# Optimization experiments

Hardware: AMD Instinct MI355X
Metric: run time of the kernel (lower is better)

The kernel has to match this reference:

```python
import jax, jax.numpy as jnp
import numpy as np

B, T, C, HEAD = 4, 4096, 1024, 64
SCALE = 1.0 / (C ** 0.5)  # module divides by embedding_size**0.5, not head_size**0.5


def setup_inputs() -> dict:
    key = jax.random.key(0)
    kx, kq, kk, kv = jax.random.split(key, 4)
    x = jax.random.normal(kx, (B, T, C), dtype=jnp.float32)
    # nn.Linear(C, head_size, bias=False) weights, stored as (C, head_size) for x @ W
    Wq = jax.random.normal(kq, (C, HEAD), dtype=jnp.float32) * (1.0 / np.sqrt(C))
    Wk = jax.random.normal(kk, (C, HEAD), dtype=jnp.float32) * (1.0 / np.sqrt(C))
    Wv = jax.random.normal(kv, (C, HEAD), dtype=jnp.float32) * (1.0 / np.sqrt(C))
    return {"x": x, "Wq": Wq, "Wk": Wk, "Wv": Wv}


def reference(x, Wq, Wk, Wv):
    q = jnp.einsum('btc,ch->bth', x, Wq)  # [B,T,HEAD]
    k = jnp.einsum('btc,ch->bth', x, Wk)
    v = jnp.einsum('btc,ch->bth', x, Wv)
    aff = jnp.einsum('bqh,bkh->bqk', q, k) * SCALE  # [B,T,T]
    causal = jnp.tril(jnp.ones((T, T), dtype=bool))
    aff = jnp.where(causal, aff, -jnp.inf)
    p = jax.nn.softmax(aff, axis=-1)  # dropout p=0.0 -> identity
    return jnp.einsum('bqk,bkh->bqh', p, v)  # [B,T,HEAD]
```

## Files before the change

kernel.cpp:

```cpp
#include <hip/hip_runtime.h>

#define T_SEQ 4096
#define NBATCH 4
#define CDIM 1024
#define NHEAD 64
#define SCALE (1.0f / 32.0f)
#define BT (NBATCH * T_SEQ)
#define NW 8

typedef __bf16 bf16x8 __attribute__((ext_vector_type(8)));
typedef float f32x4 __attribute__((ext_vector_type(4)));
typedef unsigned long long u64;

__device__ __forceinline__ unsigned short f2bf(float f) {
  union { float f; unsigned u; } x;
  x.f = f;
  unsigned r = x.u + 0x7FFFu + ((x.u >> 16) & 1u);
  return (unsigned short)(r >> 16);
}

__device__ __forceinline__ unsigned pack_bf16(float lo, float hi) {
  return (unsigned)f2bf(lo) | ((unsigned)f2bf(hi) << 16);
}

__device__ __forceinline__ f32x4 mfma16(bf16x8 a, bf16x8 b, f32x4 c) {
  return __builtin_amdgcn_mfma_f32_16x16x32_bf16(a, b, c, 0, 0, 0);
}

__device__ __forceinline__ bf16x8 ones8() {
  bf16x8 v;
  for (int j = 0; j < 8; ++j) v[j] = (__bf16)1.0f;
  return v;
}

__global__ void prep_w(const float* __restrict__ Wq, const float* __restrict__ Wk,
                       const float* __restrict__ Wv, unsigned short* __restrict__ Wt) {
  int c = blockIdx.x;
  const float* W = (c < 64) ? Wq : (c < 128) ? Wk : Wv;
  int cc = c & 63;
  float sc = (c < 64) ? SCALE : 1.0f;
  for (int k = threadIdx.x; k < CDIM; k += blockDim.x)
    Wt[c * CDIM + k] = f2bf(W[k * NHEAD + cc] * sc);
}

__global__ __launch_bounds__(256) void proj_qkv(
    const float* __restrict__ x, const unsigned short* __restrict__ Wt,
    unsigned short* __restrict__ qws, unsigned short* __restrict__ kws,
    unsigned short* __restrict__ vtws) {
  __shared__ unsigned short xlds[32][136];
  const int tid = threadIdx.x;
  const int lane = tid & 63;
  const int w = tid >> 6;
  const int g = lane >> 4;
  const int c15 = lane & 15;
  const int rb = blockIdx.x * 32;

  f32x4 acc[2][3];
  for (int i = 0; i < 2; i++)
    for (int j = 0; j < 3; j++) acc[i][j] = (f32x4){0.f, 0.f, 0.f, 0.f};

  const int sr = tid >> 3;
  const int sc = (tid & 7) * 16;
  const float* xrow = x + (size_t)(rb + sr) * CDIM + sc;

  float4 cur[4];
  for (int i = 0; i < 4; i++) cur[i] = *(const float4*)(xrow + i * 4);

  for (int k0 = 0; k0 < CDIM; k0 += 128) {
    unsigned short pk[16];
    for (int i = 0; i < 4; i++) {
      pk[i * 4 + 0] = f2bf(cur[i].x);
      pk[i * 4 + 1] = f2bf(cur[i].y);
      pk[i * 4 + 2] = f2bf(cur[i].z);
      pk[i * 4 + 3] = f2bf(cur[i].w);
    }
    *(bf16x8*)&xlds[sr][sc] = *(bf16x8*)&pk[0];
    *(bf16x8*)&xlds[sr][sc + 8] = *(bf16x8*)&pk[8];
    __syncthreads();
    if (k0 + 128 < CDIM)
      for (int i = 0; i < 4; i++)
        cur[i] = *(const float4*)(xrow + k0 + 128 + i * 4);

    for (int kk = 0; kk < 4; kk++) {
      bf16x8 a[2];
      for (int mt = 0; mt < 2; mt++)
        a[mt] = *(bf16x8*)&xlds[mt * 16 + c15][kk * 32 + g * 8];
      for (int bn = 0; bn < 3; bn++) {
        int col = w * 48 + bn * 16 + c15;
        bf16x8 bfrag =
            *(const bf16x8*)&Wt[(size_t)col * CDIM + k0 + kk * 32 + g * 8];
        for (int mt = 0; mt < 2; mt++)
          acc[mt][bn] = mfma16(a[mt], bfrag, acc[mt][bn]);
      }
    }
    __syncthreads();
  }

  for (int mt = 0; mt < 2; mt++)
    for (int bn = 0; bn < 3; bn++) {
      int col = w * 48 + bn * 16 + c15;
      int row0 = rb + mt * 16 + 4 * g;
      for (int r = 0; r < 4; r++) {
        unsigned short v = f2bf(acc[mt][bn][r]);
        int t = row0 + r;
        if (col < 64)
          qws[(size_t)t * 64 + col] = v;
        else if (col < 128)
          kws[(size_t)t * 64 + (col - 64)] = v;
        else
          vtws[(size_t)(col - 128) * BT + t] = v;
      }
    }
}

__global__ __launch_bounds__(512, 2) void attn_fwd(
    const unsigned short* __restrict__ qws, const unsigned short* __restrict__ kws,
    const unsigned short* __restrict__ vtws, float* __restrict__ out) {
  __shared__ __align__(16) char smem[NW * 8448];
  const int tid = threadIdx.x;
  const int lane = tid & 63;
  const int w = tid >> 6;
  const int g = lane >> 4;
  const int c = lane & 15;
  const int b = blockIdx.x >> 6;
  const int pi = blockIdx.x & 63;
  const size_t rowbase = (size_t)b * T_SEQ;
  char* wbase = smem + w * 8448;
  u64* pl = (u64*)wbase;
  const bf16x8 vone = ones8();

  for (int half = 0; half < 2; ++half) {
    const int qt = half ? (127 - pi) : pi;
    const int qb = qt * 32;
    const int nsteps = qt + 1;

    bf16x8 qf[2][2];
    for (int mi = 0; mi < 2; mi++)
      for (int hc = 0; hc < 2; hc++)
        qf[mi][hc] = *(const bf16x8*)&qws[(rowbase + qb + mi * 16 + c) * 64 +
                                          hc * 32 + g * 8];

    f32x4 o[2][4];
    f32x4 o5[2];
    float mrow[2];
    for (int mi = 0; mi < 2; mi++) {
      for (int nt = 0; nt < 4; nt++) o[mi][nt] = (f32x4){0.f, 0.f, 0.f, 0.f};
      o5[mi] = (f32x4){0.f, 0.f, 0.f, 0.f};
      mrow[mi] = -1e30f;
    }

    for (int st = w; st < nsteps; st += NW) {
      const int kt = st * 32;
      bf16x8 kc0[2], kc1[2], vc[4];
      for (int kn = 0; kn < 2; kn++) {
        kc0[kn] = *(const bf16x8*)&kws[(rowbase + kt + kn * 16 + c) * 64 + g * 8];
        kc1[kn] =
            *(const bf16x8*)&kws[(rowbase + kt + kn * 16 + c) * 64 + 32 + g * 8];
      }
      for (int nt = 0; nt < 4; nt++)
        vc[nt] =
            *(const bf16x8*)&vtws[(size_t)(nt * 16 + c) * BT + rowbase + kt + g * 8];

      f32x4 sv[2][2];
      for (int mi = 0; mi < 2; mi++)
        for (int kn = 0; kn < 2; kn++) {
          f32x4 z = (f32x4){0.f, 0.f, 0.f, 0.f};
          z = mfma16(kc0[kn], qf[mi][0], z);
          sv[mi][kn] = mfma16(kc1[kn], qf[mi][1], z);
        }

      if (st == nsteps - 1) {
        for (int mi = 0; mi < 2; mi++)
          for (int kn = 0; kn < 2; kn++)
            for (int r = 0; r < 4; r++) {
              int key = kt + kn * 16 + 4 * g + r;
              int qr = qb + mi * 16 + c;
              if (key > qr) sv[mi][kn][r] = -1e30f;
            }
      }

      for (int mi = 0; mi < 2; mi++) {
        float t = fmaxf(
            fmaxf(fmaxf(sv[mi][0][0], sv[mi][0][1]),
                  fmaxf(sv[mi][0][2], sv[mi][0][3])),
            fmaxf(fmaxf(sv[mi][1][0], sv[mi][1][1]),
                  fmaxf(sv[mi][1][2], sv[mi][1][3])));
        t = fmaxf(t, __shfl_xor(t, 16));
        t = fmaxf(t, __shfl_xor(t, 32));
        if (__any(t > mrow[mi] + 8.0f)) {
          float mn = fmaxf(mrow[mi], t);
          float a = __expf(mrow[mi] - mn);
          mrow[mi] = mn;
          for (int nt = 0; nt < 4; nt++) o[mi][nt] *= a;
          o5[mi] *= a;
        }
        for (int kn = 0; kn < 2; kn++)
          for (int r = 0; r < 4; r++)
            sv[mi][kn][r] = __expf(sv[mi][kn][r] - mrow[mi]);
        unsigned d0 = pack_bf16(sv[mi][0][0], sv[mi][0][1]);
        unsigned d1 = pack_bf16(sv[mi][0][2], sv[mi][0][3]);
        unsigned d2 = pack_bf16(sv[mi][1][0], sv[mi][1][1]);
        unsigned d3 = pack_bf16(sv[mi][1][2], sv[mi][1][3]);
        int row = mi * 16 + c;
        pl[row * 10 + g] = ((u64)d1 << 32) | d0;
        pl[row * 10 + 4 + g] = ((u64)d3 << 32) | d2;
      }

      asm volatile("" ::: "memory");

      for (int mi = 0; mi < 2; mi++) {
        union { u64 q[2]; bf16x8 v; } pu;
        pu.q[0] = pl[(mi * 16 + c) * 10 + 2 * g];
        pu.q[1] = pl[(mi * 16 + c) * 10 + 2 * g + 1];
        bf16x8 pa = pu.v;
        for (int nt = 0; nt < 4; nt++)
          o[mi][nt] = mfma16(vc[nt], pa, o[mi][nt]);
        o5[mi] = mfma16(vone, pa, o5[mi]);
      }
    }

    float* ow = (float*)wbase;
    float* mw = (float*)(wbase + 8192);
    float* lw = (float*)(wbase + 8320);
    for (int mi = 0; mi < 2; mi++)
      for (int nt = 0; nt < 4; nt++)
        for (int r = 0; r < 4; r++)
          ow[(mi * 16 + c) * 64 + nt * 16 + 4 * g + r] = o[mi][nt][r];
    if (g == 0)
      for (int mi = 0; mi < 2; mi++) {
        mw[mi * 16 + c] = mrow[mi];
        lw[mi * 16 + c] = o5[mi][0];
      }
    __syncthreads();

    for (int i = 0; i < 4; i++) {
      int e = tid + i * 512;
      int row = e >> 6;
      int d = e & 63;
      float M = -1e30f;
      for (int ww = 0; ww < NW; ww++)
        M = fmaxf(M, ((const float*)(smem + ww * 8448 + 8192))[row]);
      float L = 0.f, O = 0.f;
      for (int ww = 0; ww < NW; ww++) {
        float mv = ((const float*)(smem + ww * 8448 + 8192))[row];
        float f = __expf(mv - M);
        L += f * ((const float*)(smem + ww * 8448 + 8320))[row];
        O += f * ((const float*)(smem + ww * 8448))[row * 64 + d];
      }
      out[(rowbase + qb + row) * 64 + d] = O / L;
    }
    __syncthreads();
  }
}

extern "C" void kernel_launch(void* const* d_in, const int* in_sizes, int n_in,
                              void* d_out, int out_size, void* d_ws, size_t ws_size,
                              hipStream_t stream) {
  const float* x = (const float*)d_in[0];
  const float* Wq = (const float*)d_in[1];
  const float* Wk = (const float*)d_in[2];
  const float* Wv = (const float*)d_in[3];
  float* out = (float*)d_out;

  char* ws = (char*)d_ws;
  unsigned short* Wt = (unsigned short*)(ws);
  unsigned short* qws = (unsigned short*)(ws + 393216);
  unsigned short* kws = (unsigned short*)(ws + 393216 + 2097152);
  unsigned short* vtws = (unsigned short*)(ws + 393216 + 2 * 2097152);

  prep_w<<<dim3(192), dim3(256), 0, stream>>>(Wq, Wk, Wv, Wt);
  proj_qkv<<<dim3(512), dim3(256), 0, stream>>>(x, Wt, qws, kws, vtws);
  attn_fwd<<<dim3(256), dim3(512), 0, stream>>>(qws, kws, vtws, out);
}
```

Baseline: 80.25 us.

## Double attention waves per block, halve projection tile, pad LDS strides

The attention kernel now runs 16 waves per block instead of 8. This splits each query tile's KV range across more waves and merges their partial softmax states through shared memory, with the output scratch stride padded to 68 and the P-tile stride changed to 9 to reduce bank conflicts. The projection kernel processes 16 rows per block instead of 32 and launches twice as many blocks for more parallelism. The risks are a costlier cross-wave merge over 16 partials, more LDS per block, and less reuse of weight fragments in the projection.

```diff
diff --git a/kernel.cpp b/kernel.cpp
--- a/kernel.cpp
+++ b/kernel.cpp
@@ -6,7 +6,9 @@
 #define NHEAD 64
 #define SCALE (1.0f / 32.0f)
 #define BT (NBATCH * T_SEQ)
-#define NW 8
+#define NW 16
+#define WREG 8960
+#define PSTR 9
 
 typedef __bf16 bf16x8 __attribute__((ext_vector_type(8)));
 typedef float f32x4 __attribute__((ext_vector_type(4)));
@@ -47,76 +49,69 @@
     const float* __restrict__ x, const unsigned short* __restrict__ Wt,
     unsigned short* __restrict__ qws, unsigned short* __restrict__ kws,
     unsigned short* __restrict__ vtws) {
-  __shared__ unsigned short xlds[32][136];
+  __shared__ unsigned short xlds[16][136];
   const int tid = threadIdx.x;
   const int lane = tid & 63;
   const int w = tid >> 6;
   const int g = lane >> 4;
   const int c15 = lane & 15;
-  const int rb = blockIdx.x * 32;
-
-  f32x4 acc[2][3];
-  for (int i = 0; i < 2; i++)
-    for (int j = 0; j < 3; j++) acc[i][j] = (f32x4){0.f, 0.f, 0.f, 0.f};
-
-  const int sr = tid >> 3;
-  const int sc = (tid & 7) * 16;
-  const float* xrow = x + (size_t)(rb + sr) * CDIM + sc;
-
-  float4 cur[4];
-  for (int i = 0; i < 4; i++) cur[i] = *(const float4*)(xrow + i * 4);
+  const int rb = blockIdx.x * 16;
+
+  f32x4 acc[3];
+  for (int j = 0; j < 3; j++) acc[j] = (f32x4){0.f, 0.f, 0.f, 0.f};
+
+  const int sr = tid >> 4;
+  const int scc = (tid & 15) * 8;
+  const float* xrow = x + (size_t)(rb + sr) * CDIM + scc;
+
+  float4 cur[2];
+  cur[0] = *(const float4*)(xrow);
+  cur[1] = *(const float4*)(xrow + 4);
 
   for (int k0 = 0; k0 < CDIM; k0 += 128) {
-    unsigned short pk[16];
-    for (int i = 0; i < 4; i++) {
-      pk[i * 4 + 0] = f2bf(cur[i].x);
-      pk[i * 4 + 1] = f2bf(cur[i].y);
-      pk[i * 4 + 2] = f2bf(cur[i].z);
-      pk[i * 4 + 3] = f2bf(cur[i].w);
-    }
-    *(bf16x8*)&xlds[sr][sc] = *(bf16x8*)&pk[0];
-    *(bf16x8*)&xlds[sr][sc + 8] = *(bf16x8*)&pk[8];
-    __syncthreads();
-    if (k0 + 128 < CDIM)
-      for (int i = 0; i < 4; i++)
-        cur[i] = *(const float4*)(xrow + k0 + 128 + i * 4);
+    unsigned short pk[8];
+    pk[0] = f2bf(cur[0].x); pk[1] = f2bf(cur[0].y);
+    pk[2] = f2bf(cur[0].z); pk[3] = f2bf(cur[0].w);
+    pk[4] = f2bf(cur[1].x); pk[5] = f2bf(cur[1].y);
+    pk[6] = f2bf(cur[1].z); pk[7] = f2bf(cur[1].w);
+    *(bf16x8*)&xlds[sr][scc] = *(bf16x8*)pk;
+    __syncthreads();
+    if (k0 + 128 < CDIM) {
+      cur[0] = *(const float4*)(xrow + k0 + 128);
+      cur[1] = *(const float4*)(xrow + k0 + 132);
+    }
 
     for (int kk = 0; kk < 4; kk++) {
-      bf16x8 a[2];
-      for (int mt = 0; mt < 2; mt++)
-        a[mt] = *(bf16x8*)&xlds[mt * 16 + c15][kk * 32 + g * 8];
+      bf16x8 a = *(bf16x8*)&xlds[c15][kk * 32 + g * 8];
       for (int bn = 0; bn < 3; bn++) {
         int col = w * 48 + bn * 16 + c15;
         bf16x8 bfrag =
             *(const bf16x8*)&Wt[(size_t)col * CDIM + k0 + kk * 32 + g * 8];
-        for (int mt = 0; mt < 2; mt++)
-          acc[mt][bn] = mfma16(a[mt], bfrag, acc[mt][bn]);
+        acc[bn] = mfma16(a, bfrag, acc[bn]);
       }
     }
     __syncthreads();
   }
 
-  for (int mt = 0; mt < 2; mt++)
-    for (int bn = 0; bn < 3; bn++) {
-      int col = w * 48 + bn * 16 + c15;
-      int row0 = rb + mt * 16 + 4 * g;
-      for (int r = 0; r < 4; r++) {
-        unsigned short v = f2bf(acc[mt][bn][r]);
-        int t = row0 + r;
-        if (col < 64)
-          qws[(size_t)t * 64 + col] = v;
-        else if (col < 128)
-          kws[(size_t)t * 64 + (col - 64)] = v;
-        else
-          vtws[(size_t)(col - 128) * BT + t] = v;
-      }
-    }
-}
-
-__global__ __launch_bounds__(512, 2) void attn_fwd(
+  for (int bn = 0; bn < 3; bn++) {
+    int col = w * 48 + bn * 16 + c15;
+    for (int r = 0; r < 4; r++) {
+      unsigned short v = f2bf(acc[bn][r]);
+      int t = rb + 4 * g + r;
+      if (col < 64)
+        qws[(size_t)t * 64 + col] = v;
+      else if (col < 128)
+        kws[(size_t)t * 64 + (col - 64)] = v;
+      else
+        vtws[(size_t)(col - 128) * BT + t] = v;
+    }
+  }
+}
+
+__global__ __launch_bounds__(1024, 4) void attn_fwd(
     const unsigned short* __restrict__ qws, const unsigned short* __restrict__ kws,
     const unsigned short* __restrict__ vtws, float* __restrict__ out) {
-  __shared__ __align__(16) char smem[NW * 8448];
+  __shared__ __align__(16) char smem[NW * WREG];
   const int tid = threadIdx.x;
   const int lane = tid & 63;
   const int w = tid >> 6;
@@ -125,7 +120,7 @@
   const int b = blockIdx.x >> 6;
   const int pi = blockIdx.x & 63;
   const size_t rowbase = (size_t)b * T_SEQ;
-  char* wbase = smem + w * 8448;
+  char* wbase = smem + w * WREG;
   u64* pl = (u64*)wbase;
   const bf16x8 vone = ones8();
 
@@ -202,16 +197,16 @@
         unsigned d2 = pack_bf16(sv[mi][1][0], sv[mi][1][1]);
         unsigned d3 = pack_bf16(sv[mi][1][2], sv[mi][1][3]);
         int row = mi * 16 + c;
-        pl[row * 10 + g] = ((u64)d1 << 32) | d0;
-        pl[row * 10 + 4 + g] = ((u64)d3 << 32) | d2;
+        pl[row * PSTR + g] = ((u64)d1 << 32) | d0;
+        pl[row * PSTR + 4 + g] = ((u64)d3 << 32) | d2;
       }
 
       asm volatile("" ::: "memory");
 
       for (int mi = 0; mi < 2; mi++) {
         union { u64 q[2]; bf16x8 v; } pu;
-        pu.q[0] = pl[(mi * 16 + c) * 10 + 2 * g];
-        pu.q[1] = pl[(mi * 16 + c) * 10 + 2 * g + 1];
+        pu.q[0] = pl[(mi * 16 + c) * PSTR + 2 * g];
+        pu.q[1] = pl[(mi * 16 + c) * PSTR + 2 * g + 1];
         bf16x8 pa = pu.v;
         for (int nt = 0; nt < 4; nt++)
           o[mi][nt] = mfma16(vc[nt], pa, o[mi][nt]);
@@ -220,12 +215,12 @@
     }
 
     float* ow = (float*)wbase;
-    float* mw = (float*)(wbase + 8192);
-    float* lw = (float*)(wbase + 8320);
+    float* mw = (float*)(wbase + 8704);
+    float* lw = (float*)(wbase + 8832);
     for (int mi = 0; mi < 2; mi++)
       for (int nt = 0; nt < 4; nt++)
         for (int r = 0; r < 4; r++)
-          ow[(mi * 16 + c) * 64 + nt * 16 + 4 * g + r] = o[mi][nt][r];
+          ow[(mi * 16 + c) * 68 + nt * 16 + 4 * g + r] = o[mi][nt][r];
     if (g == 0)
       for (int mi = 0; mi < 2; mi++) {
         mw[mi * 16 + c] = mrow[mi];
@@ -233,19 +228,19 @@
       }
     __syncthreads();
 
-    for (int i = 0; i < 4; i++) {
-      int e = tid + i * 512;
+    for (int i = 0; i < 2; i++) {
+      int e = tid + i * 1024;
       int row = e >> 6;
       int d = e & 63;
       float M = -1e30f;
       for (int ww = 0; ww < NW; ww++)
-        M = fmaxf(M, ((const float*)(smem + ww * 8448 + 8192))[row]);
+        M = fmaxf(M, ((const float*)(smem + ww * WREG + 8704))[row]);
       float L = 0.f, O = 0.f;
       for (int ww = 0; ww < NW; ww++) {
-        float mv = ((const float*)(smem + ww * 8448 + 8192))[row];
+        float mv = ((const float*)(smem + ww * WREG + 8704))[row];
         float f = __expf(mv - M);
-        L += f * ((const float*)(smem + ww * 8448 + 8320))[row];
-        O += f * ((const float*)(smem + ww * 8448))[row * 64 + d];
+        L += f * ((const float*)(smem + ww * WREG + 8832))[row];
+        O += f * ((const float*)(smem + ww * WREG))[row * 68 + d];
       }
       out[(rowbase + qb + row) * 64 + d] = O / L;
     }
@@ -269,6 +264,6 @@
   unsigned short* vtws = (unsigned short*)(ws + 393216 + 2 * 2097152);
 
   prep_w<<<dim3(192), dim3(256), 0, stream>>>(Wq, Wk, Wv, Wt);
-  proj_qkv<<<dim3(512), dim3(256), 0, stream>>>(x, Wt, qws, kws, vtws);
-  attn_fwd<<<dim3(256), dim3(512), 0, stream>>>(qws, kws, vtws, out);
-}
+  proj_qkv<<<dim3(1024), dim3(256), 0, stream>>>(x, Wt, qws, kws, vtws);
+  attn_fwd<<<dim3(256), dim3(1024), 0, stream>>>(qws, kws, vtws, out);
+}
```

Measured after the change: 112.7 us. 40.4% more time.

## Split attention KV loop across 12 waves and pad LDS strides

Applied to the files above, without the earlier changes.

Raises the attention block from 8 to 12 waves (768 threads), so each query tile's KV range is split across more waves and combined in the final LSE merge. The per-wave LDS region is enlarged and the output staging stride is padded to 68 floats, with the P staging stride changed to 9 u64, to cut LDS bank conflicts. The aim is more latency hiding and parallelism per CU. In exchange the cross-wave merge does more work, the merge loop gets a bounds guard, and the larger block and LDS footprint may limit occupancy under the new launch bounds.

```diff
diff --git a/kernel.cpp b/kernel.cpp
--- a/kernel.cpp
+++ b/kernel.cpp
@@ -6,7 +6,9 @@
 #define NHEAD 64
 #define SCALE (1.0f / 32.0f)
 #define BT (NBATCH * T_SEQ)
-#define NW 8
+#define NW 12
+#define WREG 8960
+#define PSTR 9
 
 typedef __bf16 bf16x8 __attribute__((ext_vector_type(8)));
 typedef float f32x4 __attribute__((ext_vector_type(4)));
@@ -60,8 +62,8 @@
     for (int j = 0; j < 3; j++) acc[i][j] = (f32x4){0.f, 0.f, 0.f, 0.f};
 
   const int sr = tid >> 3;
-  const int sc = (tid & 7) * 16;
-  const float* xrow = x + (size_t)(rb + sr) * CDIM + sc;
+  const int scc = (tid & 7) * 16;
+  const float* xrow = x + (size_t)(rb + sr) * CDIM + scc;
 
   float4 cur[4];
   for (int i = 0; i < 4; i++) cur[i] = *(const float4*)(xrow + i * 4);
@@ -74,8 +76,8 @@
       pk[i * 4 + 2] = f2bf(cur[i].z);
       pk[i * 4 + 3] = f2bf(cur[i].w);
     }
-    *(bf16x8*)&xlds[sr][sc] = *(bf16x8*)&pk[0];
-    *(bf16x8*)&xlds[sr][sc + 8] = *(bf16x8*)&pk[8];
+    *(bf16x8*)&xlds[sr][scc] = *(bf16x8*)&pk[0];
+    *(bf16x8*)&xlds[sr][scc + 8] = *(bf16x8*)&pk[8];
     __syncthreads();
     if (k0 + 128 < CDIM)
       for (int i = 0; i < 4; i++)
@@ -113,10 +115,10 @@
     }
 }
 
-__global__ __launch_bounds__(512, 2) void attn_fwd(
+__global__ __launch_bounds__(768, 3) void attn_fwd(
     const unsigned short* __restrict__ qws, const unsigned short* __restrict__ kws,
     const unsigned short* __restrict__ vtws, float* __restrict__ out) {
-  __shared__ __align__(16) char smem[NW * 8448];
+  __shared__ __align__(16) char smem[NW * WREG];
   const int tid = threadIdx.x;
   const int lane = tid & 63;
   const int w = tid >> 6;
@@ -125,7 +127,7 @@
   const int b = blockIdx.x >> 6;
   const int pi = blockIdx.x & 63;
   const size_t rowbase = (size_t)b * T_SEQ;
-  char* wbase = smem + w * 8448;
+  char* wbase = smem + w * WREG;
   u64* pl = (u64*)wbase;
   const bf16x8 vone = ones8();
 
@@ -202,16 +204,16 @@
         unsigned d2 = pack_bf16(sv[mi][1][0], sv[mi][1][1]);
         unsigned d3 = pack_bf16(sv[mi][1][2], sv[mi][1][3]);
         int row = mi * 16 + c;
-        pl[row * 10 + g] = ((u64)d1 << 32) | d0;
-        pl[row * 10 + 4 + g] = ((u64)d3 << 32) | d2;
+        pl[row * PSTR + g] = ((u64)d1 << 32) | d0;
+        pl[row * PSTR + 4 + g] = ((u64)d3 << 32) | d2;
       }
 
       asm volatile("" ::: "memory");
 
       for (int mi = 0; mi < 2; mi++) {
         union { u64 q[2]; bf16x8 v; } pu;
-        pu.q[0] = pl[(mi * 16 + c) * 10 + 2 * g];
-        pu.q[1] = pl[(mi * 16 + c) * 10 + 2 * g + 1];
+        pu.q[0] = pl[(mi * 16 + c) * PSTR + 2 * g];
+        pu.q[1] = pl[(mi * 16 + c) * PSTR + 2 * g + 1];
         bf16x8 pa = pu.v;
         for (int nt = 0; nt < 4; nt++)
           o[mi][nt] = mfma16(vc[nt], pa, o[mi][nt]);
@@ -220,12 +222,12 @@
     }
 
     float* ow = (float*)wbase;
-    float* mw = (float*)(wbase + 8192);
-    float* lw = (float*)(wbase + 8320);
+    float* mw = (float*)(wbase + 8704);
+    float* lw = (float*)(wbase + 8832);
     for (int mi = 0; mi < 2; mi++)
       for (int nt = 0; nt < 4; nt++)
         for (int r = 0; r < 4; r++)
-          ow[(mi * 16 + c) * 64 + nt * 16 + 4 * g + r] = o[mi][nt][r];
+          ow[(mi * 16 + c) * 68 + nt * 16 + 4 * g + r] = o[mi][nt][r];
     if (g == 0)
       for (int mi = 0; mi < 2; mi++) {
         mw[mi * 16 + c] = mrow[mi];
@@ -233,21 +235,23 @@
       }
     __syncthreads();
 
-    for (int i = 0; i < 4; i++) {
-      int e = tid + i * 512;
-      int row = e >> 6;
-      int d = e & 63;
-      float M = -1e30f;
-      for (int ww = 0; ww < NW; ww++)
-        M = fmaxf(M, ((const float*)(smem + ww * 8448 + 8192))[row]);
-      float L = 0.f, O = 0.f;
-      for (int ww = 0; ww < NW; ww++) {
-        float mv = ((const float*)(smem + ww * 8448 + 8192))[row];
-        float f = __expf(mv - M);
-        L += f * ((const float*)(smem + ww * 8448 + 8320))[row];
-        O += f * ((const float*)(smem + ww * 8448))[row * 64 + d];
-      }
-      out[(rowbase + qb + row) * 64 + d] = O / L;
+    for (int i = 0; i < 3; i++) {
+      int e = tid + i * 768;
+      if (e < 2048) {
+        int row = e >> 6;
+        int d = e & 63;
+        float M = -1e30f;
+        for (int ww = 0; ww < NW; ww++)
+          M = fmaxf(M, ((const float*)(smem + ww * WREG + 8704))[row]);
+        float L = 0.f, O = 0.f;
+        for (int ww = 0; ww < NW; ww++) {
+          float mv = ((const float*)(smem + ww * WREG + 8704))[row];
+          float f = __expf(mv - M);
+          L += f * ((const float*)(smem + ww * WREG + 8832))[row];
+          O += f * ((const float*)(smem + ww * WREG))[row * 68 + d];
+        }
+        out[(rowbase + qb + row) * 64 + d] = O / L;
+      }
     }
     __syncthreads();
   }
@@ -270,5 +274,5 @@
 
   prep_w<<<dim3(192), dim3(256), 0, stream>>>(Wq, Wk, Wv, Wt);
   proj_qkv<<<dim3(512), dim3(256), 0, stream>>>(x, Wt, qws, kws, vtws);
-  attn_fwd<<<dim3(256), dim3(512), 0, stream>>>(qws, kws, vtws, out);
-}
+  attn_fwd<<<dim3(256), dim3(768), 0, stream>>>(qws, kws, vtws, out);
+}
```

Result: slower. 84.09 us (+4.8%).
